# Kernel tuning notes

Hardware: AMD Instinct MI355X
Metric: run time of the kernel (lower is better)

## Reference

```python
import jax, jax.numpy as jnp
import numpy as np

# q_config constants
W_IN, E_IN = 8, 4          # data_in_width, data_in_exponent_width
R_W = 6                     # data_r_width
W_OUT, E_OUT = 8, 4        # data_out_width, data_out_exponent_width (= data_n_width)
EXP_SUM_UF = 4              # exp_sum_underflow_bits
DIV_UF = 4                  # division_underflow_bits
W_DATA, E_DATA = 8, 4      # data_width, data_exponent_width

N, D = 8192, 2048


def integer_quantizer(x, width, frac_width):
    s = 2.0 ** frac_width
    lo, hi = -(2.0 ** (width - 1)), 2.0 ** (width - 1) - 1
    return jnp.clip(jnp.round(x * s), lo, hi) / s


def integer_floor_quantizer(x, width, frac_width):
    s = 2.0 ** frac_width
    lo, hi = -(2.0 ** (width - 1)), 2.0 ** (width - 1) - 1
    return jnp.clip(jnp.floor(x * s), lo, hi) / s


def mxint_quant(x, width, exponent_width):
    # MXInt block quantization with parallelism [1,1]: per-element shared exponent.
    e_hi, e_lo = 2.0 ** (exponent_width - 1) - 1, -(2.0 ** (exponent_width - 1))
    ax = jnp.abs(x)
    e = jnp.ceil(jnp.log2(jnp.where(ax == 0, 1.0, ax)))
    e = jnp.clip(e, e_lo, e_hi)
    scale = 2.0 ** (width - 1)
    m = jnp.clip(jnp.round(x * 2.0 ** (-e) * scale), -scale, scale - 1)
    qx = m * 2.0 ** e / scale
    return qx, m, e


def setup_inputs() -> dict:
    key = jax.random.key(0)
    x = jax.random.normal(key, (N, D), dtype=jnp.float32)
    return {"x": x}


def reference(x):
    # ---- MXIntHardwareExp: quantize input, range-reduce x = r + n*ln2 ----
    qx, _, _ = mxint_quant(x, W_IN, E_IN)
    log2e, _, _ = mxint_quant(jnp.float32(np.log2(np.e)), 8, 4)
    y = qx * log2e
    y = integer_floor_quantizer(y, E_OUT + R_W - 1, R_W - 1)
    n = jnp.floor(y)
    r = y - n                                # r in [0, 1)
    mexp = integer_quantizer(2.0 ** r, W_OUT, W_OUT - 2) * 2.0 ** (W_OUT - 2)
    eexp = n                                 # qexp = mexp * 2^eexp / 2^(W_OUT-2)

    # ---- exp_sum: exponent-aligned integer accumulation over dim 1 ----
    ms = (mexp * 2.0 ** EXP_SUM_UF).T        # [D, N]
    es = eexp.T                              # [D, N]

    def step(carry, me):
        out, emax = carry
        mi, ei = me
        new_emax = jnp.maximum(emax, ei)
        out = jnp.floor(out * 2.0 ** (emax - new_emax)) + jnp.floor(mi * 2.0 ** (ei - new_emax))
        return (out, new_emax), None

    (mexp_sum, eexp_sum), _ = jax.lax.scan(step, (ms[0], es[0]), (ms[1:], es[1:]))
    # mexp_sum, eexp_sum: [N]

    # ---- division: per-element mantissa integer division by the sum ----
    mout = jnp.floor(mexp * 2.0 ** (DIV_UF + EXP_SUM_UF) / mexp_sum[:, None])
    eout = eexp - eexp_sum[:, None]
    qout = mout * 2.0 ** eout / 2.0 ** DIV_UF
    qout, _, _ = mxint_quant(qout, W_DATA, E_DATA)
    return qout
```

## Files before the change

### kernel.cpp

```cpp
#include <hip/hip_runtime.h>


#define D_DIM 2048
#define TPB   256
#define EPT   8

__device__ __constant__ int c_mexp_tab[32] = {
    64, 65, 67, 68, 70, 71, 73, 74, 76, 78, 79, 81, 83, 85, 87, 89,
    91, 92, 95, 97, 99, 101, 103, 105, 108, 110, 112, 115, 117, 120, 123, 125
};

__global__ __launch_bounds__(TPB) void mxint_softmax_kernel(const float* __restrict__ x,
                                                            float* __restrict__ out) {
    const int t    = threadIdx.x;
    const int lane = t & 63;
    const int wid  = t >> 6;

    __shared__ int                s_wmax[4];
    __shared__ unsigned long long s_wsum[4];

    const int tv = c_mexp_tab[lane & 31];

    const size_t base = (size_t)blockIdx.x * D_DIM + (size_t)t * EPT;
    const float4 v0 = *(const float4*)(x + base);
    const float4 v1 = *(const float4*)(x + base + 4);
    const float xs[8] = {v0.x, v0.y, v0.z, v0.w, v1.x, v1.y, v1.z, v1.w};

    int pk[8];
    int run = -8;
#pragma unroll
    for (int j = 0; j < 8; ++j) {
        const float    xv   = xs[j];
        const unsigned bits = __float_as_uint(xv) & 0x7fffffffu;
        int e = (int)(bits >> 23) - 127 + (((bits & 0x7fffffu) != 0u) ? 1 : 0);
        e = min(7, max(-8, e));
        const float su = __uint_as_float((unsigned)(134 - e) << 23);
        int mi = (int)rintf(xv * su);
        mi = min(127, max(-128, mi));
        int yq = (mi * 46) >> (7 - e);
        yq = min(255, max(-256, yq));
        const int ee = yq >> 5;
        const int me = __builtin_amdgcn_ds_bpermute((yq & 31) << 2, tv);
        pk[j] = me | ((ee + 8) << 8);
        run   = max(run, ee);
    }

    int v = run;
#pragma unroll
    for (int d = 1; d < 64; d <<= 1) {
        const int o = __shfl_up(v, d, 64);
        if (lane >= d) v = max(v, o);
    }
    if (lane == 63) s_wmax[wid] = v;
    __syncthreads();

    int wpref = -8;
#pragma unroll
    for (int w = 0; w < 4; ++w)
        if (w < wid) wpref = max(wpref, s_wmax[w]);
    int ex = __shfl_up(v, 1, 64);
    if (lane == 0) ex = -8;
    const int P = max(wpref, ex);

    unsigned partial = 0;
    int E = P;
#pragma unroll
    for (int j = 0; j < 8; ++j) {
        const int ee = (pk[j] >> 8) - 8;
        const int me = pk[j] & 0xff;
        E = max(E, ee);
        const unsigned c = ((unsigned)me << 4) >> (E - ee);
        partial += c << (E + 8);
    }

    unsigned p32 = partial;
    p32 += __shfl_down(p32, 32, 64);
    p32 += __shfl_down(p32, 16, 64);
    p32 += __shfl_down(p32, 8, 64);
    unsigned long long p64 = p32;
    p64 += __shfl_down(p64, 4, 64);
    p64 += __shfl_down(p64, 2, 64);
    p64 += __shfl_down(p64, 1, 64);
    if (lane == 0) s_wsum[wid] = p64;
    __syncthreads();

    const unsigned long long total = s_wsum[0] + s_wsum[1] + s_wsum[2] + s_wsum[3];
    const int Estar = max(max(s_wmax[0], s_wmax[1]), max(s_wmax[2], s_wmax[3]));
    const unsigned msum = (unsigned)(total >> (Estar + 8));

    const unsigned mq    = 0x80000000u / msum;
    const unsigned mr    = 0x80000000u - mq * msum;
    const unsigned magic = (mq << 7) + ((mr << 7) / msum) + 1u;

    float res[8];
#pragma unroll
    for (int j = 0; j < 8; ++j) {
        const int      me   = pk[j] & 0xff;
        const int      ee   = (pk[j] >> 8) - 8;
        const unsigned num  = (unsigned)(me << 8);
        const unsigned mout = (unsigned)(((unsigned long long)num * magic) >> 38);
        const int eout = ee - Estar;
        const int bl   = 32 - __clz((int)(mout | 1u));
        const int pw2  = ((mout & (mout - 1u)) == 0u) ? 1 : 0;
        const int clog = bl - pw2;
        const int s    = min(7 - clog, eout + 11);
        const int rs   = 8 - s;
        const unsigned u    = mout << 8;
        const unsigned bse  = u >> rs;
        const unsigned frac = u & ((1u << rs) - 1u);
        const unsigned half = 1u << (rs - 1);
        unsigned m2 = bse + (((frac > half) || (frac == half && (bse & 1u))) ? 1u : 0u);
        m2 = min(m2, 127u);
        const int ef = max(clog + eout - 4, -8);
        res[j] = (float)m2 * __uint_as_float((unsigned)(ef + 120) << 23);
    }

    const float4 out0 = {res[0], res[1], res[2], res[3]};
    const float4 out1 = {res[4], res[5], res[6], res[7]};
    *(float4*)(out + base)     = out0;
    *(float4*)(out + base + 4) = out1;
}

extern "C" void kernel_launch(void* const* d_in, const int* in_sizes, int n_in,
                              void* d_out, int out_size, void* d_ws, size_t ws_size,
                              hipStream_t stream) {
    const float* x   = (const float*)d_in[0];
    float*       o   = (float*)d_out;
    const int rows = in_sizes[0] / D_DIM;
    mxint_softmax_kernel<<<rows, TPB, 0, stream>>>(x, o);
}
```

Before: 121.2 us.

## Map one wavefront per row and use an LDS lookup table for output quantization

Each 64-lane wavefront now handles a whole row, 32 elements per lane, and four rows share a block. This removes the block-wide __syncthreads and the shared-memory cross-wave reductions. The exponent-aligned accumulation becomes a chunked prefix-max scan with a carried running maximum. The per-element output requantization is replaced by a 512-entry LDS table indexed by (exponent difference, mantissa quotient), and the reciprocal magic number is computed with a double division. In exchange, each lane holds more registers and runs eight wave scans instead of one, and the table is rebuilt by every wave.

```diff
diff --git a/kernel.cpp b/kernel.cpp
--- a/kernel.cpp
+++ b/kernel.cpp
@@ -3,7 +3,7 @@
 
 #define D_DIM 2048
 #define TPB   256
-#define EPT   8
+#define RPB   4
 
 __device__ __constant__ int c_mexp_tab[32] = {
     64, 65, 67, 68, 70, 71, 73, 74, 76, 78, 79, 81, 83, 85, 87, 89,
@@ -15,117 +15,119 @@
     const int t    = threadIdx.x;
     const int lane = t & 63;
     const int wid  = t >> 6;
+    const int row  = blockIdx.x * RPB + wid;
 
-    __shared__ int                s_wmax[4];
-    __shared__ unsigned long long s_wsum[4];
+    __shared__ float s_res[RPB][512];
+    float* wt = s_res[wid];
+
+#pragma unroll
+    for (int q = 0; q < 8; ++q) {
+        const int      idx   = q * 64 + lane;
+        const unsigned mout  = (unsigned)(idx & 31);
+        const int      eoutn = idx >> 5;
+        const int      bl    = 32 - __clz((int)(mout | 1u));
+        const int      pw2   = ((mout & (mout - 1u)) == 0u) ? 1 : 0;
+        const int      clog  = bl - pw2;
+        const int      s     = min(7 - clog, 11 - eoutn);
+        const int      rs    = 8 - s;
+        const unsigned u     = mout << 8;
+        const unsigned bse   = u >> rs;
+        const unsigned frac  = u & ((1u << rs) - 1u);
+        const unsigned half  = 1u << (rs - 1);
+        unsigned m2 = bse + (((frac > half) || (frac == half && (bse & 1u))) ? 1u : 0u);
+        m2 = min(m2, 127u);
+        const int ef = max(clog - eoutn - 4, -8);
+        wt[idx] = (float)m2 * __uint_as_float((unsigned)(ef + 120) << 23);
+    }
 
     const int tv = c_mexp_tab[lane & 31];
 
-    const size_t base = (size_t)blockIdx.x * D_DIM + (size_t)t * EPT;
-    const float4 v0 = *(const float4*)(x + base);
-    const float4 v1 = *(const float4*)(x + base + 4);
-    const float xs[8] = {v0.x, v0.y, v0.z, v0.w, v1.x, v1.y, v1.z, v1.w};
+    const float* xr = x + (size_t)row * D_DIM;
+    float4 v[8];
+#pragma unroll
+    for (int i = 0; i < 8; ++i)
+        v[i] = *(const float4*)(xr + i * 256 + lane * 4);
 
-    int pk[8];
-    int run = -8;
+    unsigned pk[16];
+    unsigned partial = 0;
+    int carry8 = 0;
+
 #pragma unroll
-    for (int j = 0; j < 8; ++j) {
-        const float    xv   = xs[j];
-        const unsigned bits = __float_as_uint(xv) & 0x7fffffffu;
-        int e = (int)(bits >> 23) - 127 + (((bits & 0x7fffffu) != 0u) ? 1 : 0);
-        e = min(7, max(-8, e));
-        const float su = __uint_as_float((unsigned)(134 - e) << 23);
-        int mi = (int)rintf(xv * su);
-        mi = min(127, max(-128, mi));
-        int yq = (mi * 46) >> (7 - e);
-        yq = min(255, max(-256, yq));
-        const int ee = yq >> 5;
-        const int me = __builtin_amdgcn_ds_bpermute((yq & 31) << 2, tv);
-        pk[j] = me | ((ee + 8) << 8);
-        run   = max(run, ee);
+    for (int i = 0; i < 8; ++i) {
+        const float xs4[4] = {v[i].x, v[i].y, v[i].z, v[i].w};
+        int me[4], e8[4], a[4];
+#pragma unroll
+        for (int k = 0; k < 4; ++k) {
+            const float    xv   = xs4[k];
+            const unsigned bits = __float_as_uint(xv) & 0x7fffffffu;
+            const int      eb   = (int)((bits + 0x7fffffu) >> 23);
+            const int      ebc  = min(134, max(119, eb));
+            const float    su   = __uint_as_float((unsigned)(261 - ebc) << 23);
+            int mi = (int)rintf(xv * su);
+            mi = min(127, max(-128, mi));
+            int yq = (mi * 46) >> (134 - ebc);
+            yq = min(255, max(-256, yq));
+            e8[k] = (yq >> 5) + 8;
+            me[k] = __builtin_amdgcn_ds_bpermute((yq & 31) << 2, tv);
+            a[k]  = (k == 0) ? e8[0] : max(a[k - 1], e8[k]);
+        }
+
+        int sc = a[3];
+#pragma unroll
+        for (int d = 1; d < 64; d <<= 1) {
+            const int o = __shfl_up(sc, d, 64);
+            if (lane >= d) sc = max(sc, o);
+        }
+        int ex = __shfl_up(sc, 1, 64);
+        if (lane == 0) ex = 0;
+        const int base = max(carry8, ex);
+
+#pragma unroll
+        for (int k = 0; k < 4; ++k) {
+            const int E8 = max(base, a[k]);
+            const unsigned c = ((unsigned)me[k] << 4) >> (E8 - e8[k]);
+            partial += c << E8;
+        }
+        pk[2 * i]     = (unsigned)me[0] | ((unsigned)e8[0] << 8)
+                      | ((unsigned)me[1] << 16) | ((unsigned)e8[1] << 24);
+        pk[2 * i + 1] = (unsigned)me[2] | ((unsigned)e8[2] << 8)
+                      | ((unsigned)me[3] << 16) | ((unsigned)e8[3] << 24);
+
+        carry8 = max(carry8, __shfl(sc, 63, 64));
     }
 
-    int v = run;
+    unsigned long long p64 = partial;
 #pragma unroll
-    for (int d = 1; d < 64; d <<= 1) {
-        const int o = __shfl_up(v, d, 64);
-        if (lane >= d) v = max(v, o);
+    for (int d = 32; d >= 1; d >>= 1) p64 += __shfl_xor(p64, d, 64);
+
+    const int      Estar8 = carry8;
+    const unsigned msum   = (unsigned)(p64 >> Estar8);
+    const unsigned magic  = (unsigned)(274877906944.0 / (double)msum) + 1u;
+
+    float* orow = out + (size_t)row * D_DIM;
+#pragma unroll
+    for (int i = 0; i < 8; ++i) {
+        float r4[4];
+#pragma unroll
+        for (int k = 0; k < 4; ++k) {
+            const unsigned p   = pk[2 * i + (k >> 1)];
+            const unsigned sh  = (unsigned)(k & 1) * 16u;
+            const unsigned mel = (p >> sh) & 0xffu;
+            const unsigned ee8 = (p >> (sh + 8)) & 0xffu;
+            const unsigned mout  = __umulhi(mel << 8, magic) >> 6;
+            const int      eoutn = Estar8 - (int)ee8;
+            r4[k] = wt[(eoutn << 5) | (int)mout];
+        }
+        const float4 o4 = {r4[0], r4[1], r4[2], r4[3]};
+        *(float4*)(orow + i * 256 + lane * 4) = o4;
     }
-    if (lane == 63) s_wmax[wid] = v;
-    __syncthreads();
-
-    int wpref = -8;
-#pragma unroll
-    for (int w = 0; w < 4; ++w)
-        if (w < wid) wpref = max(wpref, s_wmax[w]);
-    int ex = __shfl_up(v, 1, 64);
-    if (lane == 0) ex = -8;
-    const int P = max(wpref, ex);
-
-    unsigned partial = 0;
-    int E = P;
-#pragma unroll
-    for (int j = 0; j < 8; ++j) {
-        const int ee = (pk[j] >> 8) - 8;
-        const int me = pk[j] & 0xff;
-        E = max(E, ee);
-        const unsigned c = ((unsigned)me << 4) >> (E - ee);
-        partial += c << (E + 8);
-    }
-
-    unsigned p32 = partial;
-    p32 += __shfl_down(p32, 32, 64);
-    p32 += __shfl_down(p32, 16, 64);
-    p32 += __shfl_down(p32, 8, 64);
-    unsigned long long p64 = p32;
-    p64 += __shfl_down(p64, 4, 64);
-    p64 += __shfl_down(p64, 2, 64);
-    p64 += __shfl_down(p64, 1, 64);
-    if (lane == 0) s_wsum[wid] = p64;
-    __syncthreads();
-
-    const unsigned long long total = s_wsum[0] + s_wsum[1] + s_wsum[2] + s_wsum[3];
-    const int Estar = max(max(s_wmax[0], s_wmax[1]), max(s_wmax[2], s_wmax[3]));
-    const unsigned msum = (unsigned)(total >> (Estar + 8));
-
-    const unsigned mq    = 0x80000000u / msum;
-    const unsigned mr    = 0x80000000u - mq * msum;
-    const unsigned magic = (mq << 7) + ((mr << 7) / msum) + 1u;
-
-    float res[8];
-#pragma unroll
-    for (int j = 0; j < 8; ++j) {
-        const int      me   = pk[j] & 0xff;
-        const int      ee   = (pk[j] >> 8) - 8;
-        const unsigned num  = (unsigned)(me << 8);
-        const unsigned mout = (unsigned)(((unsigned long long)num * magic) >> 38);
-        const int eout = ee - Estar;
-        const int bl   = 32 - __clz((int)(mout | 1u));
-        const int pw2  = ((mout & (mout - 1u)) == 0u) ? 1 : 0;
-        const int clog = bl - pw2;
-        const int s    = min(7 - clog, eout + 11);
-        const int rs   = 8 - s;
-        const unsigned u    = mout << 8;
-        const unsigned bse  = u >> rs;
-        const unsigned frac = u & ((1u << rs) - 1u);
-        const unsigned half = 1u << (rs - 1);
-        unsigned m2 = bse + (((frac > half) || (frac == half && (bse & 1u))) ? 1u : 0u);
-        m2 = min(m2, 127u);
-        const int ef = max(clog + eout - 4, -8);
-        res[j] = (float)m2 * __uint_as_float((unsigned)(ef + 120) << 23);
-    }
-
-    const float4 out0 = {res[0], res[1], res[2], res[3]};
-    const float4 out1 = {res[4], res[5], res[6], res[7]};
-    *(float4*)(out + base)     = out0;
-    *(float4*)(out + base + 4) = out1;
 }
 
 extern "C" void kernel_launch(void* const* d_in, const int* in_sizes, int n_in,
                               void* d_out, int out_size, void* d_ws, size_t ws_size,
                               hipStream_t stream) {
-    const float* x   = (const float*)d_in[0];
-    float*       o   = (float*)d_out;
+    const float* x = (const float*)d_in[0];
+    float*       o = (float*)d_out;
     const int rows = in_sizes[0] / D_DIM;
-    mxint_softmax_kernel<<<rows, TPB, 0, stream>>>(x, o);
+    mxint_softmax_kernel<<<rows / RPB, TPB, 0, stream>>>(x, o);
 }
```

New measurement: 114.1 us. 5.9% less time.
